# Kernel tuning notes

Measured on AMD Instinct MI355X. Metric: run time of the kernel, lower is better.

Reference implementation:

```python
import jax, jax.numpy as jnp
import numpy as np

L, B, S, C, H, V = 12, 2, 1024, 768, 12, 50257
D = C // H
FF = 4 * C
SCALE = 1.0 / float(np.sqrt(D))


def setup_inputs() -> dict:
    key = jax.random.key(0)
    ks = jax.random.split(key, 10)
    s = 0.02  # GPT-2 init std
    return {
        "idx": jax.random.randint(ks[0], (B, S), 0, V),
        "targets": jax.random.randint(ks[1], (B, S), 0, V),
        "wte": jax.random.normal(ks[2], (V, C), jnp.float32) * s,
        "wpe": jax.random.normal(ks[3], (S, C), jnp.float32) * s,
        "ln1_w": jnp.ones((L, C), jnp.float32),
        "ln1_b": jnp.zeros((L, C), jnp.float32),
        "qkv_w": jax.random.normal(ks[4], (L, C, 3 * C), jnp.float32) * s,
        "qkv_b": jnp.zeros((L, 3 * C), jnp.float32),
        "proj_w": jax.random.normal(ks[5], (L, C, C), jnp.float32) * s,
        "proj_b": jnp.zeros((L, C), jnp.float32),
        "ln2_w": jnp.ones((L, C), jnp.float32),
        "ln2_b": jnp.zeros((L, C), jnp.float32),
        "fc_w": jax.random.normal(ks[6], (L, C, FF), jnp.float32) * s,
        "fc_b": jnp.zeros((L, FF), jnp.float32),
        "fc2_w": jax.random.normal(ks[7], (L, FF, C), jnp.float32) * s,
        "fc2_b": jnp.zeros((L, C), jnp.float32),
        "lnf_w": jnp.ones((C,), jnp.float32),
        "lnf_b": jnp.zeros((C,), jnp.float32),
    }


def _ln(x, w, b):
    m = jnp.mean(x, axis=-1, keepdims=True)
    v = jnp.mean(jnp.square(x - m), axis=-1, keepdims=True)
    return (x - m) * jax.lax.rsqrt(v + 1e-5) * w + b


def _gpt(wte, wpe, ln1_w, ln1_b, qkv_w, qkv_b, proj_w, proj_b,
         ln2_w, ln2_b, fc_w, fc_b, fc2_w, fc2_b, lnf_w, lnf_b, idx, targets):
    h = wte[idx] + wpe[jnp.arange(S)]  # [B,S,C]
    causal = jnp.tril(jnp.ones((S, S), bool))

    def block(h, p):
        l1w, l1b, qw, qb, pw, pb, l2w, l2b, fw, fb, gw, gb = p
        x = _ln(h, l1w, l1b)
        q, k, v = jnp.split(x @ qw + qb, 3, axis=-1)  # each [B,S,C]
        heads = lambda t: t.reshape(B, S, H, D).transpose(0, 2, 1, 3)  # [B,H,S,D]
        q, k, v = heads(q), heads(k), heads(v)
        scores = jnp.einsum('bhsd,bhtd->bhst', q, k) * SCALE
        scores = jnp.where(causal, scores, -jnp.inf)
        att = jax.nn.softmax(scores, axis=-1)
        o = jnp.einsum('bhst,bhtd->bhsd', att, v)
        o = o.transpose(0, 2, 1, 3).reshape(B, S, C)
        h = h + o @ pw + pb
        x = _ln(h, l2w, l2b)
        h = h + jax.nn.gelu(x @ fw + fb, approximate=True) @ gw + gb
        return h, None

    h, _ = jax.lax.scan(block, h, (ln1_w, ln1_b, qkv_w, qkv_b, proj_w, proj_b,
                                   ln2_w, ln2_b, fc_w, fc_b, fc2_w, fc2_b))
    logits = _ln(h, lnf_w, lnf_b) @ wte.T  # tied lm_head, [B,S,V]
    logp = jax.nn.log_softmax(logits, axis=-1)
    loss = -jnp.mean(jnp.take_along_axis(logp, targets[..., None], axis=-1))
    return logits, loss


def reference(idx, targets, wte, wpe, ln1_w, ln1_b, qkv_w, qkv_b, proj_w, proj_b,
              ln2_w, ln2_b, fc_w, fc_b, fc2_w, fc2_b, lnf_w, lnf_b):
    return _gpt(wte, wpe, ln1_w, ln1_b, qkv_w, qkv_b, proj_w, proj_b,
                ln2_w, ln2_b, fc_w, fc_b, fc2_w, fc2_b, lnf_w, lnf_b, idx, targets)
```

## Files before the change

kernel.cpp:

```cpp
#include <hip/hip_runtime.h>
#include <hip/hip_bf16.h>
#include <cstdint>
#include <cstddef>

constexpr int LNUM = 12;
constexpr int BB   = 2;
constexpr int SS   = 1024;
constexpr int CC   = 768;
constexpr int HH   = 12;
constexpr int DD   = 64;
constexpr int FFD  = 3072;
constexpr int VV   = 50257;
constexpr int VPAD = 50304;
constexpr int NBX  = VPAD / 128;
constexpr int MM   = BB * SS;

typedef unsigned short u16;
typedef short     s16x8 __attribute__((ext_vector_type(8)));
typedef float     f32x4 __attribute__((ext_vector_type(4)));
typedef u16       u16x4 __attribute__((ext_vector_type(4)));
typedef u16       u16x8 __attribute__((ext_vector_type(8)));

__device__ __forceinline__ float bf2f(u16 v) {
    return __uint_as_float(((unsigned)v) << 16);
}
__device__ __forceinline__ u16 f2bf(float f) {
    unsigned u = __float_as_uint(f);
    return (u16)((u + 0x7fffu + ((u >> 16) & 1u)) >> 16);
}


__global__ __launch_bounds__(256) void wte_conv_kernel(const float* __restrict__ wte,
                                                       u16* __restrict__ out) {
    size_t i4 = ((size_t)blockIdx.x * 256 + threadIdx.x) * 4;
    if (i4 >= (size_t)VPAD * CC) return;
    size_t r = i4 / CC;
    u16x4 o;
    if (r < (size_t)VV) {
        const float4 v = *(const float4*)&wte[i4];
        o[0] = f2bf(v.x); o[1] = f2bf(v.y); o[2] = f2bf(v.z); o[3] = f2bf(v.w);
    } else {
        o[0] = o[1] = o[2] = o[3] = 0;
    }
    *(u16x4*)&out[i4] = o;
}

__global__ __launch_bounds__(256) void transpose_conv_kernel(const float* __restrict__ in,
                                                             u16* __restrict__ out,
                                                             int R, int Cn) {
    __shared__ float tile[32][33];
    const float* inp = in + (size_t)blockIdx.z * R * Cn;
    u16* outp = out + (size_t)blockIdx.z * R * Cn;
    int c  = blockIdx.x * 32 + threadIdx.x;
    int r0 = blockIdx.y * 32;
#pragma unroll
    for (int i = 0; i < 4; ++i) {
        int r = r0 + threadIdx.y + i * 8;
        tile[threadIdx.y + i * 8][threadIdx.x] = inp[(size_t)r * Cn + c];
    }
    __syncthreads();
    int oc = r0 + threadIdx.x;
#pragma unroll
    for (int i = 0; i < 4; ++i) {
        int orow = blockIdx.x * 32 + threadIdx.y + i * 8;
        outp[(size_t)orow * R + oc] = f2bf(tile[threadIdx.x][threadIdx.y + i * 8]);
    }
}

__global__ __launch_bounds__(256) void embed_kernel(const int* __restrict__ idx,
                                                    const float* __restrict__ wte,
                                                    const float* __restrict__ wpe,
                                                    float* __restrict__ h) {
    int row = blockIdx.x;
    int s   = row & (SS - 1);
    int tok = idx[row];
    const float* we = wte + (size_t)tok * CC;
    const float* pe = wpe + (size_t)s * CC;
    float* hr = h + (size_t)row * CC;
    for (int c = threadIdx.x; c < CC; c += 256) hr[c] = we[c] + pe[c];
}

__global__ __launch_bounds__(256) void ln_kernel(const float* __restrict__ h,
                                                 const float* __restrict__ w,
                                                 const float* __restrict__ b,
                                                 u16* __restrict__ x) {
    int row = blockIdx.x, tid = threadIdx.x;
    const float* hr = h + (size_t)row * CC;
    float v0 = hr[tid], v1 = hr[tid + 256], v2 = hr[tid + 512];
    float s  = v0 + v1 + v2;
    float s2 = v0 * v0 + v1 * v1 + v2 * v2;
#pragma unroll
    for (int off = 32; off; off >>= 1) {
        s  += __shfl_xor(s, off);
        s2 += __shfl_xor(s2, off);
    }
    __shared__ float rs[4], rs2[4], stat[2];
    int wid = tid >> 6;
    if ((tid & 63) == 0) { rs[wid] = s; rs2[wid] = s2; }
    __syncthreads();
    if (tid == 0) {
        float ts  = rs[0] + rs[1] + rs[2] + rs[3];
        float ts2 = rs2[0] + rs2[1] + rs2[2] + rs2[3];
        float mean = ts * (1.0f / CC);
        float var  = ts2 * (1.0f / CC) - mean * mean;
        stat[0] = mean;
        stat[1] = rsqrtf(var + 1e-5f);
    }
    __syncthreads();
    float mean = stat[0], rstd = stat[1];
    size_t base = (size_t)row * CC;
    x[base + tid]       = f2bf((v0 - mean) * rstd * w[tid]       + b[tid]);
    x[base + tid + 256] = f2bf((v1 - mean) * rstd * w[tid + 256] + b[tid + 256]);
    x[base + tid + 512] = f2bf((v2 - mean) * rstd * w[tid + 512] + b[tid + 512]);
}

template <int BM, int BN, int EPI>
__global__ __launch_bounds__(256)
void gemm_bt_kernel(const u16* __restrict__ A, const u16* __restrict__ Bt,
                    const float* __restrict__ bias, float* __restrict__ outf,
                    u16* __restrict__ outb, int K, long long ldo,
                    float* __restrict__ partM, float* __restrict__ partS) {
    constexpr int MR  = BM / 32, NR = BN / 32;
    constexpr int ACH = BM * 64 / (256 * 8);
    constexpr int BCH = BN * 64 / (256 * 8);
    __shared__ u16 As[BM * 64];
    __shared__ u16 Bs[BN * 64];
    const int tid  = threadIdx.x;
    const int lane = tid & 63;
    const int wid  = tid >> 6;
    const int l15  = lane & 15;
    const int lq   = lane >> 4;
    const int wm   = wid & 1;
    const int wn   = wid >> 1;
    const int rx   = l15 & 7;

    const int gx = gridDim.x, gy = gridDim.y;
    const int nwg = gx * gy;
    const int pos = blockIdx.y * gx + blockIdx.x;
    const int qc  = nwg >> 3, rc = nwg & 7;
    const int xcd = pos & 7, cidx = pos >> 3;
    const int wgid = (xcd < rc ? xcd * (qc + 1) : rc * (qc + 1) + (xcd - rc) * qc) + cidx;
    const int bx = wgid / gy, by = wgid % gy;
    const int bm0 = by * BM, bn0 = bx * BN;

    f32x4 acc[MR][NR];
#pragma unroll
    for (int m = 0; m < MR; ++m)
#pragma unroll
        for (int n = 0; n < NR; ++n) acc[m][n] = (f32x4){0.f, 0.f, 0.f, 0.f};

    u16x8 areg[ACH], breg[BCH];
    auto ldreg = [&](int kt) {
#pragma unroll
        for (int it = 0; it < ACH; ++it) {
            int g = it * 256 + tid, r = g >> 3, c = ((g & 7) ^ (r & 7)) * 8;
            areg[it] = *(const u16x8*)&A[(size_t)(bm0 + r) * (size_t)K + kt + c];
        }
#pragma unroll
        for (int it = 0; it < BCH; ++it) {
            int g = it * 256 + tid, r = g >> 3, c = ((g & 7) ^ (r & 7)) * 8;
            breg[it] = *(const u16x8*)&Bt[(size_t)(bn0 + r) * (size_t)K + kt + c];
        }
    };
    auto wlds = [&]() {
#pragma unroll
        for (int it = 0; it < ACH; ++it) *(u16x8*)&As[(it * 256 + tid) * 8] = areg[it];
#pragma unroll
        for (int it = 0; it < BCH; ++it) *(u16x8*)&Bs[(it * 256 + tid) * 8] = breg[it];
    };
    auto compute = [&]() {
#pragma unroll
        for (int ks = 0; ks < 2; ++ks) {
            s16x8 af[MR], bfr[NR];
#pragma unroll
            for (int m = 0; m < MR; ++m) {
                int row = wm * (BM / 2) + m * 16 + l15;
                af[m] = *(const s16x8*)&As[row * 64 + (((ks * 4 + lq) ^ rx) * 8)];
            }
#pragma unroll
            for (int n = 0; n < NR; ++n) {
                int row = wn * (BN / 2) + n * 16 + l15;
                bfr[n] = *(const s16x8*)&Bs[row * 64 + (((ks * 4 + lq) ^ rx) * 8)];
            }
#pragma unroll
            for (int m = 0; m < MR; ++m)
#pragma unroll
                for (int n = 0; n < NR; ++n)
                    acc[m][n] = __builtin_amdgcn_mfma_f32_16x16x32_bf16(af[m], bfr[n], acc[m][n], 0, 0, 0);
        }
    };

    const int nk = K >> 6;
    ldreg(0);
    for (int t = 0; t < nk; ++t) {
        __syncthreads();
        wlds();
        __syncthreads();
        if (t + 1 < nk) ldreg((t + 1) << 6);
        compute();
    }

#pragma unroll
    for (int m = 0; m < MR; ++m) {
#pragma unroll
        for (int n = 0; n < NR; ++n) {
#pragma unroll
            for (int r = 0; r < 4; ++r) {
                int row = bm0 + wm * (BM / 2) + m * 16 + lq * 4 + r;
                int col = bn0 + wn * (BN / 2) + n * 16 + l15;
                float v = acc[m][n][r];
                if (EPI != 3) v += bias[col];
                if (EPI == 1) {
                    float xg = v;
                    v = 0.5f * xg * (1.0f + tanhf(0.7978845608028654f * (xg + 0.044715f * xg * xg * xg)));
                }
                if (EPI == 0 || EPI == 1) {
                    outb[(size_t)row * ldo + col] = f2bf(v);
                } else if (EPI == 2) {
                    outf[(size_t)row * ldo + col] += v;
                } else {
                    if (col < VV) outf[(size_t)row * ldo + col] = v;
                }
            }
        }
    }

    if constexpr (EPI == 3) {
        __shared__ float redM[2][BM], redS[2][BM];
#pragma unroll
        for (int m = 0; m < MR; ++m) {
#pragma unroll
            for (int r = 0; r < 4; ++r) {
                float mx = -3.0e38f;
#pragma unroll
                for (int n = 0; n < NR; ++n) {
                    int colg = bn0 + wn * (BN / 2) + n * 16 + l15;
                    float v = (colg < VV) ? acc[m][n][r] : -3.0e38f;
                    mx = fmaxf(mx, v);
                }
#pragma unroll
                for (int off = 1; off < 16; off <<= 1) mx = fmaxf(mx, __shfl_xor(mx, off));
                float sm = 0.f;
#pragma unroll
                for (int n = 0; n < NR; ++n) {
                    int colg = bn0 + wn * (BN / 2) + n * 16 + l15;
                    if (colg < VV) sm += __expf(acc[m][n][r] - mx);
                }
#pragma unroll
                for (int off = 1; off < 16; off <<= 1) sm += __shfl_xor(sm, off);
                if (l15 == 0) {
                    int rl = wm * (BM / 2) + m * 16 + lq * 4 + r;
                    redM[wn][rl] = mx;
                    redS[wn][rl] = sm;
                }
            }
        }
        __syncthreads();
        if (tid < BM) {
            float m0 = redM[0][tid], m1 = redM[1][tid];
            float M = fmaxf(m0, m1);
            float S = redS[0][tid] * __expf(m0 - M) + redS[1][tid] * __expf(m1 - M);
            size_t rowg = (size_t)(bm0 + tid);
            partM[rowg * NBX + bx] = M;
            partS[rowg * NBX + bx] = S;
        }
    }
}

__global__ __launch_bounds__(256) void vtrans_kernel(const u16* __restrict__ qkv,
                                                     u16* __restrict__ vT) {
    __shared__ u16 T[64 * 64];
    const int tid = threadIdx.x;
    const int t0  = blockIdx.x * 64;
    const int bh  = blockIdx.y;
    const int b   = bh / HH, hh = bh % HH;
    const u16* vp = qkv + (size_t)b * SS * (3 * CC) + 2 * CC + hh * DD;
#pragma unroll
    for (int it = 0; it < 2; ++it) {
        int g = it * 256 + tid;
        int t = g >> 3, dg = g & 7;
        u16x8 v = *(const u16x8*)&vp[(size_t)(t0 + t) * (3 * CC) + dg * 8];
        *(u16x8*)&T[(t * 8 + (dg ^ (t & 7))) * 8] = v;
    }
    __syncthreads();
    u16* op = vT + (size_t)bh * DD * SS + t0;
#pragma unroll
    for (int it = 0; it < 2; ++it) {
        int g = it * 256 + tid;
        int d = g >> 3, tc = g & 7;
        u16x8 o;
#pragma unroll
        for (int e = 0; e < 8; ++e) {
            int t = tc * 8 + e;
            o[e] = T[(t * 8 + ((d >> 3) ^ (t & 7))) * 8 + (d & 7)];
        }
        *(u16x8*)&op[(size_t)d * SS + tc * 8] = o;
    }
}

__global__ __launch_bounds__(256) void attn_mfma3_kernel(const u16* __restrict__ qkv,
                                                         const u16* __restrict__ vT,
                                                         u16* __restrict__ o) {
    constexpr int PADC = 72;
    __shared__ u16 Ks[64][PADC];
    __shared__ u16 Vs[64][PADC];
    __shared__ u16 Ps[4][16][PADC];

    const int tid = threadIdx.x, lane = tid & 63, wid = tid >> 6;
    const int l15 = lane & 15, lq = lane >> 4;
    const int pos = blockIdx.x;
    const int j   = 15 - pos / 24;
    const int bh  = pos % 24;
    const int b   = bh / HH, hh = bh % HH;
    const int q0  = j * 64;

    const size_t base = (size_t)b * SS * (3 * CC);
    const u16* kp = qkv + base + CC + hh * DD;
    const u16* vp = vT + (size_t)bh * DD * SS;

    s16x8 qf[2];
    {
        const u16* qr = qkv + base + hh * DD + (size_t)(q0 + wid * 16 + l15) * (3 * CC);
        qf[0] = *(const s16x8*)&qr[lq * 8];
        qf[1] = *(const s16x8*)&qr[32 + lq * 8];
    }

    float m[4], lsum[4];
    f32x4 acc_o[4];
#pragma unroll
    for (int r = 0; r < 4; ++r) { m[r] = -3.0e38f; lsum[r] = 0.f; }
#pragma unroll
    for (int nd = 0; nd < 4; ++nd) acc_o[nd] = (f32x4){0.f, 0.f, 0.f, 0.f};

    for (int tt = 0; tt <= j; ++tt) {
        const int t0 = tt * 64;
        __syncthreads();
#pragma unroll
        for (int it = 0; it < 2; ++it) {
            int g = it * 256 + tid;
            int r = g >> 3, c = (g & 7) * 8;
            *(u16x8*)&Ks[r][c] = *(const u16x8*)&kp[(size_t)(t0 + r) * (3 * CC) + c];
            *(u16x8*)&Vs[r][c] = *(const u16x8*)&vp[(size_t)r * SS + t0 + c];
        }
        __syncthreads();

        f32x4 sc[4];
#pragma unroll
        for (int n = 0; n < 4; ++n) sc[n] = (f32x4){0.f, 0.f, 0.f, 0.f};
#pragma unroll
        for (int ks = 0; ks < 2; ++ks) {
#pragma unroll
            for (int n = 0; n < 4; ++n) {
                s16x8 kb = *(const s16x8*)&Ks[n * 16 + l15][ks * 32 + lq * 8];
                sc[n] = __builtin_amdgcn_mfma_f32_16x16x32_bf16(qf[ks], kb, sc[n], 0, 0, 0);
            }
        }

        if (tt == j) {
#pragma unroll
            for (int n = 0; n < 4; ++n) {
                int colg = t0 + n * 16 + l15;
#pragma unroll
                for (int r = 0; r < 4; ++r) {
                    int rowg = q0 + wid * 16 + lq * 4 + r;
                    float sv = sc[n][r] * 0.125f;
                    sc[n][r] = (colg <= rowg) ? sv : -3.0e38f;
                }
            }
        } else {
#pragma unroll
            for (int n = 0; n < 4; ++n)
#pragma unroll
                for (int r = 0; r < 4; ++r) sc[n][r] *= 0.125f;
        }

        float mt[4];
#pragma unroll
        for (int r = 0; r < 4; ++r)
            mt[r] = fmaxf(fmaxf(sc[0][r], sc[1][r]), fmaxf(sc[2][r], sc[3][r]));
#pragma unroll
        for (int off = 1; off < 16; off <<= 1)
#pragma unroll
            for (int r = 0; r < 4; ++r) mt[r] = fmaxf(mt[r], __shfl_xor(mt[r], off));
        float rs[4];
#pragma unroll
        for (int r = 0; r < 4; ++r) {
            float mn  = fmaxf(m[r], mt[r]);
            float scl = __expf(m[r] - mn);
            m[r] = mn;
            float ps = 0.f;
#pragma unroll
            for (int n = 0; n < 4; ++n) {
                float p = __expf(sc[n][r] - mn);
                sc[n][r] = p;
                ps += p;
            }
            rs[r] = ps;
            lsum[r] *= scl;
#pragma unroll
            for (int nd = 0; nd < 4; ++nd) acc_o[nd][r] *= scl;
        }
#pragma unroll
        for (int off = 1; off < 16; off <<= 1)
#pragma unroll
            for (int r = 0; r < 4; ++r) rs[r] += __shfl_xor(rs[r], off);
#pragma unroll
        for (int r = 0; r < 4; ++r) lsum[r] += rs[r];

#pragma unroll
        for (int n = 0; n < 4; ++n)
#pragma unroll
            for (int r = 0; r < 4; ++r)
                Ps[wid][lq * 4 + r][n * 16 + l15] = f2bf(sc[n][r]);

#pragma unroll
        for (int ks = 0; ks < 2; ++ks) {
            s16x8 pa = *(const s16x8*)&Ps[wid][l15][ks * 32 + lq * 8];
#pragma unroll
            for (int nd = 0; nd < 4; ++nd) {
                s16x8 vb = *(const s16x8*)&Vs[nd * 16 + l15][ks * 32 + lq * 8];
                acc_o[nd] = __builtin_amdgcn_mfma_f32_16x16x32_bf16(pa, vb, acc_o[nd], 0, 0, 0);
            }
        }
    }

#pragma unroll
    for (int r = 0; r < 4; ++r) {
        float inv = 1.f / lsum[r];
        int rowg = q0 + wid * 16 + lq * 4 + r;
        u16* orow = o + ((size_t)b * SS + rowg) * CC + hh * DD;
#pragma unroll
        for (int nd = 0; nd < 4; ++nd)
            orow[nd * 16 + l15] = f2bf(acc_o[nd][r] * inv);
    }
}

__global__ __launch_bounds__(256) void lse_kernel(const float* __restrict__ partM,
                                                  const float* __restrict__ partS,
                                                  const float* __restrict__ logits,
                                                  const int* __restrict__ tgt,
                                                  float* __restrict__ lossp) {
    int row = blockIdx.x, tid = threadIdx.x;
    float m = -3.0e38f, s = 0.f;
    for (int i = tid; i < NBX; i += 256) {
        float pm = partM[(size_t)row * NBX + i];
        float ps = partS[(size_t)row * NBX + i];
        float nm = fmaxf(m, pm);
        s = s * __expf(m - nm) + ps * __expf(pm - nm);
        m = nm;
    }
#pragma unroll
    for (int off = 32; off; off >>= 1) {
        float om = __shfl_xor(m, off), os = __shfl_xor(s, off);
        float nm = fmaxf(m, om);
        s = s * __expf(m - nm) + os * __expf(om - nm);
        m = nm;
    }
    __shared__ float rm[4], rsh[4];
    int wid = tid >> 6;
    if ((tid & 63) == 0) { rm[wid] = m; rsh[wid] = s; }
    __syncthreads();
    if (tid == 0) {
        float M = fmaxf(fmaxf(rm[0], rm[1]), fmaxf(rm[2], rm[3]));
        float S = rsh[0] * __expf(rm[0] - M) + rsh[1] * __expf(rm[1] - M) +
                  rsh[2] * __expf(rm[2] - M) + rsh[3] * __expf(rm[3] - M);
        float lse = M + __logf(S);
        lossp[row] = lse - logits[(size_t)row * VV + tgt[row]];
    }
}

__global__ __launch_bounds__(256) void loss_reduce_kernel(const float* __restrict__ lossp,
                                                          float* __restrict__ out) {
    int tid = threadIdx.x;
    float s = 0.f;
    for (int i = tid; i < MM; i += 256) s += lossp[i];
#pragma unroll
    for (int off = 32; off; off >>= 1) s += __shfl_xor(s, off);
    __shared__ float r[4];
    if ((tid & 63) == 0) r[tid >> 6] = s;
    __syncthreads();
    if (tid == 0) out[0] = (r[0] + r[1] + r[2] + r[3]) * (1.0f / MM);
}

extern "C" void kernel_launch(void* const* d_in, const int* in_sizes, int n_in,
                              void* d_out, int out_size, void* d_ws, size_t ws_size,
                              hipStream_t stream) {
    const int*   idx     = (const int*)  d_in[0];
    const int*   targets = (const int*)  d_in[1];
    const float* wte     = (const float*)d_in[2];
    const float* wpe     = (const float*)d_in[3];
    const float* ln1w    = (const float*)d_in[4];
    const float* ln1b    = (const float*)d_in[5];
    const float* qkvw    = (const float*)d_in[6];
    const float* qkvbi   = (const float*)d_in[7];
    const float* projw   = (const float*)d_in[8];
    const float* projbi  = (const float*)d_in[9];
    const float* ln2w    = (const float*)d_in[10];
    const float* ln2b    = (const float*)d_in[11];
    const float* fcw     = (const float*)d_in[12];
    const float* fcbi    = (const float*)d_in[13];
    const float* fc2w    = (const float*)d_in[14];
    const float* fc2bi   = (const float*)d_in[15];
    const float* lnfw    = (const float*)d_in[16];
    const float* lnfb    = (const float*)d_in[17];
    float* logits = (float*)d_out;

    char* wsb = (char*)d_ws;
    size_t off = 0;
    auto alloc = [&](size_t n) -> char* {
        char* p = wsb + off;
        off = (off + n + 255) & ~(size_t)255;
        return p;
    };
    u16*   wteT  = (u16*)  alloc((size_t)VPAD * CC * 2);
    u16*   qkvT  = (u16*)  alloc((size_t)LNUM * 3 * CC * CC * 2);
    u16*   projT = (u16*)  alloc((size_t)LNUM * CC * CC * 2);
    u16*   fcT   = (u16*)  alloc((size_t)LNUM * FFD * CC * 2);
    u16*   fc2T  = (u16*)  alloc((size_t)LNUM * CC * FFD * 2);
    float* h     = (float*)alloc((size_t)MM * CC * 4);
    u16*   xb    = (u16*)  alloc((size_t)MM * CC * 2);
    u16*   qkvb  = (u16*)  alloc((size_t)MM * 3 * CC * 2);
    u16*   ob    = (u16*)  alloc((size_t)MM * CC * 2);
    u16*   gb    = (u16*)  alloc((size_t)MM * FFD * 2);
    u16*   vTb   = (u16*)  alloc((size_t)BB * HH * DD * SS * 2);
    float* lossp = (float*)alloc((size_t)MM * 4);
    float* partM = (float*)alloc((size_t)MM * NBX * 4);
    float* partS = (float*)alloc((size_t)MM * NBX * 4);

    {
        int blocks = (int)(((size_t)VPAD * CC / 4 + 255) / 256);
        wte_conv_kernel<<<blocks, 256, 0, stream>>>(wte, wteT);
    }
    transpose_conv_kernel<<<dim3(3 * CC / 32, CC / 32, LNUM), dim3(32, 8), 0, stream>>>(qkvw, qkvT, CC, 3 * CC);
    transpose_conv_kernel<<<dim3(CC / 32, CC / 32, LNUM),     dim3(32, 8), 0, stream>>>(projw, projT, CC, CC);
    transpose_conv_kernel<<<dim3(FFD / 32, CC / 32, LNUM),    dim3(32, 8), 0, stream>>>(fcw, fcT, CC, FFD);
    transpose_conv_kernel<<<dim3(CC / 32, FFD / 32, LNUM),    dim3(32, 8), 0, stream>>>(fc2w, fc2T, FFD, CC);

    embed_kernel<<<MM, 256, 0, stream>>>(idx, wte, wpe, h);

    for (int l = 0; l < LNUM; ++l) {
        const u16* qkvT_l  = qkvT  + (size_t)l * 3 * CC * CC;
        const u16* projT_l = projT + (size_t)l * CC * CC;
        const u16* fcT_l   = fcT   + (size_t)l * FFD * CC;
        const u16* fc2T_l  = fc2T  + (size_t)l * CC * FFD;

        ln_kernel<<<MM, 256, 0, stream>>>(h, ln1w + (size_t)l * CC, ln1b + (size_t)l * CC, xb);
        gemm_bt_kernel<128, 128, 0><<<dim3(3 * CC / 128, MM / 128), 256, 0, stream>>>(
            xb, qkvT_l, qkvbi + (size_t)l * 3 * CC, nullptr, qkvb, CC, 3 * CC, nullptr, nullptr);
        vtrans_kernel<<<dim3(SS / 64, BB * HH), 256, 0, stream>>>(qkvb, vTb);
        attn_mfma3_kernel<<<BB * HH * 16, 256, 0, stream>>>(qkvb, vTb, ob);
        gemm_bt_kernel<64, 64, 2><<<dim3(CC / 64, MM / 64), 256, 0, stream>>>(
            ob, projT_l, projbi + (size_t)l * CC, h, nullptr, CC, CC, nullptr, nullptr);
        ln_kernel<<<MM, 256, 0, stream>>>(h, ln2w + (size_t)l * CC, ln2b + (size_t)l * CC, xb);
        gemm_bt_kernel<128, 128, 1><<<dim3(FFD / 128, MM / 128), 256, 0, stream>>>(
            xb, fcT_l, fcbi + (size_t)l * FFD, nullptr, gb, CC, FFD, nullptr, nullptr);
        gemm_bt_kernel<64, 64, 2><<<dim3(CC / 64, MM / 64), 256, 0, stream>>>(
            gb, fc2T_l, fc2bi + (size_t)l * CC, h, nullptr, FFD, CC, nullptr, nullptr);
    }

    ln_kernel<<<MM, 256, 0, stream>>>(h, lnfw, lnfb, xb);
    gemm_bt_kernel<128, 128, 3><<<dim3(VPAD / 128, MM / 128), 256, 0, stream>>>(
        xb, wteT, nullptr, logits, nullptr, CC, VV, partM, partS);

    lse_kernel<<<MM, 256, 0, stream>>>(partM, partS, logits, targets, lossp);
    loss_reduce_kernel<<<1, 256, 0, stream>>>(lossp, logits + (size_t)MM * VV);
}
```

Before: 2.052 ms.

## Fuse LayerNorm into following GEMMs via residual-epilogue row statistics

Removes the two per-layer LayerNorm kernels. The residual-add GEMM epilogues and the embedding kernel now accumulate per-row sum and sum of squares with atomics. The QKV and FC GEMMs read fp32 h directly and normalize it on the fly while loading the A tile. This saves 24 kernel launches and the bf16 write and re-read of the normalized activation. In exchange the A loads double in bytes, each N-tile block recomputes the normalization, and the one-pass variance from atomics may lose some precision.

```diff
diff --git a/kernel.cpp b/kernel.cpp
--- a/kernel.cpp
+++ b/kernel.cpp
@@ -70,14 +70,34 @@
 __global__ __launch_bounds__(256) void embed_kernel(const int* __restrict__ idx,
                                                     const float* __restrict__ wte,
                                                     const float* __restrict__ wpe,
-                                                    float* __restrict__ h) {
+                                                    float* __restrict__ h,
+                                                    float* __restrict__ stats0) {
     int row = blockIdx.x;
+    int tid = threadIdx.x;
     int s   = row & (SS - 1);
     int tok = idx[row];
     const float* we = wte + (size_t)tok * CC;
     const float* pe = wpe + (size_t)s * CC;
     float* hr = h + (size_t)row * CC;
-    for (int c = threadIdx.x; c < CC; c += 256) hr[c] = we[c] + pe[c];
+    float sm = 0.f, sq = 0.f;
+    for (int c = tid; c < CC; c += 256) {
+        float v = we[c] + pe[c];
+        hr[c] = v;
+        sm += v; sq += v * v;
+    }
+#pragma unroll
+    for (int off = 32; off; off >>= 1) {
+        sm += __shfl_xor(sm, off);
+        sq += __shfl_xor(sq, off);
+    }
+    __shared__ float rs[4], rs2[4];
+    int wid = tid >> 6;
+    if ((tid & 63) == 0) { rs[wid] = sm; rs2[wid] = sq; }
+    __syncthreads();
+    if (tid == 0) {
+        stats0[row * 2]     = rs[0] + rs[1] + rs[2] + rs[3];
+        stats0[row * 2 + 1] = rs2[0] + rs2[1] + rs2[2] + rs2[3];
+    }
 }
 
 __global__ __launch_bounds__(256) void ln_kernel(const float* __restrict__ h,
@@ -114,11 +134,15 @@
     x[base + tid + 512] = f2bf((v2 - mean) * rstd * w[tid + 512] + b[tid + 512]);
 }
 
-template <int BM, int BN, int EPI>
+template <int BM, int BN, int EPI, bool LNA>
 __global__ __launch_bounds__(256)
-void gemm_bt_kernel(const u16* __restrict__ A, const u16* __restrict__ Bt,
-                    const float* __restrict__ bias, float* __restrict__ outf,
-                    u16* __restrict__ outb, int K, long long ldo,
+void gemm_bt_kernel(const u16* __restrict__ Ab, const float* __restrict__ Af,
+                    const float* __restrict__ Ast,
+                    const float* __restrict__ lnw, const float* __restrict__ lnb,
+                    const u16* __restrict__ Bt, const float* __restrict__ bias,
+                    float* __restrict__ outf, u16* __restrict__ outb,
+                    float* __restrict__ stats_out,
+                    int K, long long ldo,
                     float* __restrict__ partM, float* __restrict__ partS) {
     constexpr int MR  = BM / 32, NR = BN / 32;
     constexpr int ACH = BM * 64 / (256 * 8);
@@ -149,12 +173,45 @@
 #pragma unroll
         for (int n = 0; n < NR; ++n) acc[m][n] = (f32x4){0.f, 0.f, 0.f, 0.f};
 
+    float meanv[LNA ? ACH : 1], rstdv[LNA ? ACH : 1];
+    if constexpr (LNA) {
+#pragma unroll
+        for (int it = 0; it < ACH; ++it) {
+            int r = (it * 256 + tid) >> 3;
+            float sum = Ast[(bm0 + r) * 2], ssq = Ast[(bm0 + r) * 2 + 1];
+            float mean = sum * (1.0f / CC);
+            meanv[it] = mean;
+            rstdv[it] = rsqrtf(ssq * (1.0f / CC) - mean * mean + 1e-5f);
+        }
+    }
+
     u16x8 areg[ACH], breg[BCH];
     auto ldreg = [&](int kt) {
 #pragma unroll
         for (int it = 0; it < ACH; ++it) {
             int g = it * 256 + tid, r = g >> 3, c = ((g & 7) ^ (r & 7)) * 8;
-            areg[it] = *(const u16x8*)&A[(size_t)(bm0 + r) * (size_t)K + kt + c];
+            if constexpr (LNA) {
+                const float* hp = &Af[(size_t)(bm0 + r) * (size_t)K + kt + c];
+                float4 h0 = *(const float4*)hp;
+                float4 h1 = *(const float4*)(hp + 4);
+                const float* wp = &lnw[kt + c];
+                const float* bp = &lnb[kt + c];
+                float4 w0 = *(const float4*)wp, w1 = *(const float4*)(wp + 4);
+                float4 b0 = *(const float4*)bp, b1 = *(const float4*)(bp + 4);
+                float mean = meanv[it], rstd = rstdv[it];
+                u16x8 pk;
+                pk[0] = f2bf((h0.x - mean) * rstd * w0.x + b0.x);
+                pk[1] = f2bf((h0.y - mean) * rstd * w0.y + b0.y);
+                pk[2] = f2bf((h0.z - mean) * rstd * w0.z + b0.z);
+                pk[3] = f2bf((h0.w - mean) * rstd * w0.w + b0.w);
+                pk[4] = f2bf((h1.x - mean) * rstd * w1.x + b1.x);
+                pk[5] = f2bf((h1.y - mean) * rstd * w1.y + b1.y);
+                pk[6] = f2bf((h1.z - mean) * rstd * w1.z + b1.z);
+                pk[7] = f2bf((h1.w - mean) * rstd * w1.w + b1.w);
+                areg[it] = pk;
+            } else {
+                areg[it] = *(const u16x8*)&Ab[(size_t)(bm0 + r) * (size_t)K + kt + c];
+            }
         }
 #pragma unroll
         for (int it = 0; it < BCH; ++it) {
@@ -200,6 +257,7 @@
         compute();
     }
 
+    float hv[EPI == 2 ? MR : 1][EPI == 2 ? NR : 1][4];
 #pragma unroll
     for (int m = 0; m < MR; ++m) {
 #pragma unroll
@@ -217,9 +275,33 @@
                 if (EPI == 0 || EPI == 1) {
                     outb[(size_t)row * ldo + col] = f2bf(v);
                 } else if (EPI == 2) {
-                    outf[(size_t)row * ldo + col] += v;
+                    float nh = outf[(size_t)row * ldo + col] + v;
+                    outf[(size_t)row * ldo + col] = nh;
+                    hv[m][n][r] = nh;
                 } else {
                     if (col < VV) outf[(size_t)row * ldo + col] = v;
+                }
+            }
+        }
+    }
+
+    if constexpr (EPI == 2) {
+#pragma unroll
+        for (int m = 0; m < MR; ++m) {
+#pragma unroll
+            for (int r = 0; r < 4; ++r) {
+                float p = 0.f, p2 = 0.f;
+#pragma unroll
+                for (int n = 0; n < NR; ++n) { p += hv[m][n][r]; p2 += hv[m][n][r] * hv[m][n][r]; }
+#pragma unroll
+                for (int off = 1; off < 16; off <<= 1) {
+                    p  += __shfl_xor(p, off);
+                    p2 += __shfl_xor(p2, off);
+                }
+                if (l15 == 0) {
+                    int row = bm0 + wm * (BM / 2) + m * 16 + lq * 4 + r;
+                    atomicAdd(&stats_out[row * 2], p);
+                    atomicAdd(&stats_out[row * 2 + 1], p2);
                 }
             }
         }
@@ -526,6 +608,10 @@
     float* lossp = (float*)alloc((size_t)MM * 4);
     float* partM = (float*)alloc((size_t)MM * NBX * 4);
     float* partS = (float*)alloc((size_t)MM * NBX * 4);
+    float* ln1st = (float*)alloc((size_t)(LNUM + 1) * MM * 2 * 4);
+    float* ln2st = (float*)alloc((size_t)LNUM * MM * 2 * 4);
+
+    hipMemsetAsync(ln1st, 0, (size_t)(2 * LNUM + 1) * MM * 2 * 4, stream);
 
     {
         int blocks = (int)(((size_t)VPAD * CC / 4 + 255) / 256);
@@ -536,31 +622,42 @@
     transpose_conv_kernel<<<dim3(FFD / 32, CC / 32, LNUM),    dim3(32, 8), 0, stream>>>(fcw, fcT, CC, FFD);
     transpose_conv_kernel<<<dim3(CC / 32, FFD / 32, LNUM),    dim3(32, 8), 0, stream>>>(fc2w, fc2T, FFD, CC);
 
-    embed_kernel<<<MM, 256, 0, stream>>>(idx, wte, wpe, h);
+    embed_kernel<<<MM, 256, 0, stream>>>(idx, wte, wpe, h, ln1st);
 
     for (int l = 0; l < LNUM; ++l) {
         const u16* qkvT_l  = qkvT  + (size_t)l * 3 * CC * CC;
         const u16* projT_l = projT + (size_t)l * CC * CC;
         const u16* fcT_l   = fcT   + (size_t)l * FFD * CC;
         const u16* fc2T_l  = fc2T  + (size_t)l * CC * FFD;
-
-        ln_kernel<<<MM, 256, 0, stream>>>(h, ln1w + (size_t)l * CC, ln1b + (size_t)l * CC, xb);
-        gemm_bt_kernel<128, 128, 0><<<dim3(3 * CC / 128, MM / 128), 256, 0, stream>>>(
-            xb, qkvT_l, qkvbi + (size_t)l * 3 * CC, nullptr, qkvb, CC, 3 * CC, nullptr, nullptr);
+        float* ln1st_l = ln1st + (size_t)l * MM * 2;
+        float* ln2st_l = ln2st + (size_t)l * MM * 2;
+
+        gemm_bt_kernel<128, 128, 0, true><<<dim3(3 * CC / 128, MM / 128), 256, 0, stream>>>(
+            nullptr, h, ln1st_l, ln1w + (size_t)l * CC, ln1b + (size_t)l * CC,
+            qkvT_l, qkvbi + (size_t)l * 3 * CC, nullptr, qkvb, nullptr,
+            CC, 3 * CC, nullptr, nullptr);
         vtrans_kernel<<<dim3(SS / 64, BB * HH), 256, 0, stream>>>(qkvb, vTb);
         attn_mfma3_kernel<<<BB * HH * 16, 256, 0, stream>>>(qkvb, vTb, ob);
-        gemm_bt_kernel<64, 64, 2><<<dim3(CC / 64, MM / 64), 256, 0, stream>>>(
-            ob, projT_l, projbi + (size_t)l * CC, h, nullptr, CC, CC, nullptr, nullptr);
-        ln_kernel<<<MM, 256, 0, stream>>>(h, ln2w + (size_t)l * CC, ln2b + (size_t)l * CC, xb);
-        gemm_bt_kernel<128, 128, 1><<<dim3(FFD / 128, MM / 128), 256, 0, stream>>>(
-            xb, fcT_l, fcbi + (size_t)l * FFD, nullptr, gb, CC, FFD, nullptr, nullptr);
-        gemm_bt_kernel<64, 64, 2><<<dim3(CC / 64, MM / 64), 256, 0, stream>>>(
-            gb, fc2T_l, fc2bi + (size_t)l * CC, h, nullptr, FFD, CC, nullptr, nullptr);
+        gemm_bt_kernel<64, 64, 2, false><<<dim3(CC / 64, MM / 64), 256, 0, stream>>>(
+            ob, nullptr, nullptr, nullptr, nullptr,
+            projT_l, projbi + (size_t)l * CC, h, nullptr, ln2st_l,
+            CC, CC, nullptr, nullptr);
+        gemm_bt_kernel<128, 128, 1, true><<<dim3(FFD / 128, MM / 128), 256, 0, stream>>>(
+            nullptr, h, ln2st_l, ln2w + (size_t)l * CC, ln2b + (size_t)l * CC,
+            fcT_l, fcbi + (size_t)l * FFD, nullptr, gb, nullptr,
+            CC, FFD, nullptr, nullptr);
+        gemm_bt_kernel<64, 64, 2, false><<<dim3(CC / 64, MM / 64), 256, 0, stream>>>(
+            gb, nullptr, nullptr, nullptr, nullptr,
+            fc2T_l, fc2bi + (size_t)l * CC, h, nullptr,
+            ln1st + (size_t)(l + 1) * MM * 2,
+            FFD, CC, nullptr, nullptr);
     }
 
     ln_kernel<<<MM, 256, 0, stream>>>(h, lnfw, lnfb, xb);
-    gemm_bt_kernel<128, 128, 3><<<dim3(VPAD / 128, MM / 128), 256, 0, stream>>>(
-        xb, wteT, nullptr, logits, nullptr, CC, VV, partM, partS);
+    gemm_bt_kernel<128, 128, 3, false><<<dim3(VPAD / 128, MM / 128), 256, 0, stream>>>(
+        xb, nullptr, nullptr, nullptr, nullptr,
+        wteT, nullptr, logits, nullptr, nullptr,
+        CC, VV, partM, partS);
 
     lse_kernel<<<MM, 256, 0, stream>>>(partM, partS, logits, targets, lossp);
     loss_reduce_kernel<<<1, 256, 0, stream>>>(lossp, logits + (size_t)MM * VV);
```

Result: slower. 2.340 ms (+14.1%).

## Prefetch next K/V tile into registers in attention; cheaper GELU via exp

Applied to the files above, without the earlier changes.

The attention loop now loads the next 64-row K and V tiles from global memory into registers while the current tile is being computed. The registers are written to shared memory at the start of the next iteration, so global load latency overlaps with the MFMA and softmax work. Separately, the tanh-approximate GELU in the FC epilogue is rewritten as x/(1+exp(-2z)), which is mathematically equivalent and replaces tanhf with the faster __expf intrinsic. The prefetch costs extra registers per thread, which may reduce occupancy.

```diff
diff --git a/kernel.cpp b/kernel.cpp
--- a/kernel.cpp
+++ b/kernel.cpp
@@ -211,8 +211,8 @@
                 float v = acc[m][n][r];
                 if (EPI != 3) v += bias[col];
                 if (EPI == 1) {
-                    float xg = v;
-                    v = 0.5f * xg * (1.0f + tanhf(0.7978845608028654f * (xg + 0.044715f * xg * xg * xg)));
+                    float z = 0.7978845608028654f * (v + 0.044715f * v * v * v);
+                    v = v / (1.0f + __expf(-2.0f * z));
                 }
                 if (EPI == 0 || EPI == 1) {
                     outb[(size_t)row * ldo + col] = f2bf(v);
@@ -332,30 +332,39 @@
 #pragma unroll
     for (int nd = 0; nd < 4; ++nd) acc_o[nd] = (f32x4){0.f, 0.f, 0.f, 0.f};
 
+    const int sr = tid >> 3, sc = (tid & 7) * 8;
+    const int sr1 = sr + 32;
+    u16x8 kreg[2], vreg[2];
+    auto ldkv = [&](int t0) {
+        kreg[0] = *(const u16x8*)&kp[(size_t)(t0 + sr) * (3 * CC) + sc];
+        vreg[0] = *(const u16x8*)&vp[(size_t)sr * SS + t0 + sc];
+        kreg[1] = *(const u16x8*)&kp[(size_t)(t0 + sr1) * (3 * CC) + sc];
+        vreg[1] = *(const u16x8*)&vp[(size_t)sr1 * SS + t0 + sc];
+    };
+
+    ldkv(0);
     for (int tt = 0; tt <= j; ++tt) {
-        const int t0 = tt * 64;
         __syncthreads();
-#pragma unroll
-        for (int it = 0; it < 2; ++it) {
-            int g = it * 256 + tid;
-            int r = g >> 3, c = (g & 7) * 8;
-            *(u16x8*)&Ks[r][c] = *(const u16x8*)&kp[(size_t)(t0 + r) * (3 * CC) + c];
-            *(u16x8*)&Vs[r][c] = *(const u16x8*)&vp[(size_t)r * SS + t0 + c];
-        }
+        *(u16x8*)&Ks[sr][sc]  = kreg[0];
+        *(u16x8*)&Vs[sr][sc]  = vreg[0];
+        *(u16x8*)&Ks[sr1][sc] = kreg[1];
+        *(u16x8*)&Vs[sr1][sc] = vreg[1];
         __syncthreads();
-
-        f32x4 sc[4];
-#pragma unroll
-        for (int n = 0; n < 4; ++n) sc[n] = (f32x4){0.f, 0.f, 0.f, 0.f};
+        if (tt < j) ldkv((tt + 1) * 64);
+
+        f32x4 sc4[4];
+#pragma unroll
+        for (int n = 0; n < 4; ++n) sc4[n] = (f32x4){0.f, 0.f, 0.f, 0.f};
 #pragma unroll
         for (int ks = 0; ks < 2; ++ks) {
 #pragma unroll
             for (int n = 0; n < 4; ++n) {
                 s16x8 kb = *(const s16x8*)&Ks[n * 16 + l15][ks * 32 + lq * 8];
-                sc[n] = __builtin_amdgcn_mfma_f32_16x16x32_bf16(qf[ks], kb, sc[n], 0, 0, 0);
-            }
-        }
-
+                sc4[n] = __builtin_amdgcn_mfma_f32_16x16x32_bf16(qf[ks], kb, sc4[n], 0, 0, 0);
+            }
+        }
+
+        const int t0 = tt * 64;
         if (tt == j) {
 #pragma unroll
             for (int n = 0; n < 4; ++n) {
@@ -363,21 +372,21 @@
 #pragma unroll
                 for (int r = 0; r < 4; ++r) {
                     int rowg = q0 + wid * 16 + lq * 4 + r;
-                    float sv = sc[n][r] * 0.125f;
-                    sc[n][r] = (colg <= rowg) ? sv : -3.0e38f;
+                    float sv = sc4[n][r] * 0.125f;
+                    sc4[n][r] = (colg <= rowg) ? sv : -3.0e38f;
                 }
             }
         } else {
 #pragma unroll
             for (int n = 0; n < 4; ++n)
 #pragma unroll
-                for (int r = 0; r < 4; ++r) sc[n][r] *= 0.125f;
+                for (int r = 0; r < 4; ++r) sc4[n][r] *= 0.125f;
         }
 
         float mt[4];
 #pragma unroll
         for (int r = 0; r < 4; ++r)
-            mt[r] = fmaxf(fmaxf(sc[0][r], sc[1][r]), fmaxf(sc[2][r], sc[3][r]));
+            mt[r] = fmaxf(fmaxf(sc4[0][r], sc4[1][r]), fmaxf(sc4[2][r], sc4[3][r]));
 #pragma unroll
         for (int off = 1; off < 16; off <<= 1)
 #pragma unroll
@@ -391,8 +400,8 @@
             float ps = 0.f;
 #pragma unroll
             for (int n = 0; n < 4; ++n) {
-                float p = __expf(sc[n][r] - mn);
-                sc[n][r] = p;
+                float p = __expf(sc4[n][r] - mn);
+                sc4[n][r] = p;
                 ps += p;
             }
             rs[r] = ps;
@@ -411,7 +420,7 @@
         for (int n = 0; n < 4; ++n)
 #pragma unroll
             for (int r = 0; r < 4; ++r)
-                Ps[wid][lq * 4 + r][n * 16 + l15] = f2bf(sc[n][r]);
+                Ps[wid][lq * 4 + r][n * 16 + l15] = f2bf(sc4[n][r]);
 
 #pragma unroll
         for (int ks = 0; ks < 2; ++ks) {
```

Measured after the change: 1.990 ms. 1.03x faster.
